# Kernel tuning notes

Measured on AMD Instinct MI355X. Metric: run time of the kernel, lower is better.

## Reference

```python
import jax, jax.numpy as jnp
import numpy as np

WIN = 9
EPS = 1e-05


def _box_sum(x, win):
    """Depthwise win x win box-filter sum with SAME padding, via two separable 1D convs."""
    C = x.shape[1]
    pad = win // 2
    dn = ('NCHW', 'OIHW', 'NCHW')
    kh = jnp.ones((C, 1, win, 1), dtype=x.dtype)
    kw = jnp.ones((C, 1, 1, win), dtype=x.dtype)
    x = jax.lax.conv_general_dilated(x, kh, (1, 1), [(pad, pad), (0, 0)],
                                     dimension_numbers=dn, feature_group_count=C)
    x = jax.lax.conv_general_dilated(x, kw, (1, 1), [(0, 0), (pad, pad)],
                                     dimension_numbers=dn, feature_group_count=C)
    return x


def setup_inputs() -> dict:
    key = jax.random.key(0)
    k1, k2 = jax.random.split(key)
    B, C, H, W = 32, 4, 512, 512
    y_pred = jax.random.uniform(k1, (B, C, H, W), dtype=jnp.float32)
    y_true = jax.random.uniform(k2, (B, C, H, W), dtype=jnp.float32)
    return {"y_pred": y_pred, "y_true": y_true}


def reference(y_pred, y_true):
    C = y_true.shape[1]
    n = float(WIN * WIN)
    # Stack the 5 moment maps along channels -> one fused box-filter pass.
    stacked = jnp.concatenate(
        [y_true, y_pred, y_true * y_true, y_pred * y_pred, y_true * y_pred], axis=1)
    sums = _box_sum(stacked, WIN)
    sum_I, sum_J, sum_I2, sum_J2, sum_IJ = jnp.split(sums, 5, axis=1)
    mu_I = sum_I / n
    mu_J = sum_J / n
    var_I = sum_I2 / n - mu_I * mu_I
    var_J = sum_J2 / n - mu_J * mu_J
    cov_IJ = sum_IJ / n - mu_I * mu_J
    cc = cov_IJ * cov_IJ / (jnp.maximum(var_I, 0.0) * jnp.maximum(var_J, 0.0) + EPS)
    return -jnp.mean(cc)
```

## Files before the change

### kernel.cpp

```cpp
#include <hip/hip_runtime.h>


#define PAD 4
#define EPS 1e-5f

constexpr int B = 32, C = 4, H = 512, W = 512;
constexpr int ROWS = 16;
constexpr int NCHUNK = H / ROWS;
constexpr int NTASK = B * C * NCHUNK;
constexpr int TPB = 256;
constexpr int WPB = TPB / 64;
constexpr int NBLK = NTASK / WPB;
constexpr float INV_N = 1.0f / 81.0f;

__device__ __forceinline__ void loadrow(const float* __restrict__ p, int r,
                                        int x0, float4& a, float4& b) {
    const float* q = p + (size_t)r * W + x0;
    a = *(const float4*)q;
    b = *(const float4*)(q + 4);
}

template <int SGN>
__device__ __forceinline__ void fold8(float s[5][8],
                                      const float4& i0, const float4& i1,
                                      const float4& j0, const float4& j1) {
    const float fi[8] = {i0.x, i0.y, i0.z, i0.w, i1.x, i1.y, i1.z, i1.w};
    const float fj[8] = {j0.x, j0.y, j0.z, j0.w, j1.x, j1.y, j1.z, j1.w};
#pragma unroll
    for (int k = 0; k < 8; ++k) {
        const float a = fi[k], b = fj[k];
        if (SGN > 0) {
            s[0][k] += a; s[1][k] += b;
            s[2][k] += a * a; s[3][k] += b * b; s[4][k] += a * b;
        } else {
            s[0][k] -= a; s[1][k] -= b;
            s[2][k] -= a * a; s[3][k] -= b * b; s[4][k] -= a * b;
        }
    }
}

template <int HALF>
__device__ __forceinline__ void hsum4(const float sc[8], int lane, float h[4]) {
    float v[12];
    if (HALF == 0) {
#pragma unroll
        for (int k = 0; k < 4; ++k) {
            const float t = __shfl_up(sc[4 + k], 1, 64);
            v[k] = (lane == 0) ? 0.0f : t;
        }
#pragma unroll
        for (int k = 0; k < 8; ++k) v[4 + k] = sc[k];
    } else {
#pragma unroll
        for (int k = 0; k < 8; ++k) v[k] = sc[k];
#pragma unroll
        for (int k = 0; k < 4; ++k) {
            const float t = __shfl_down(sc[k], 1, 64);
            v[8 + k] = (lane == 63) ? 0.0f : t;
        }
    }
    float t = v[0] + v[1] + v[2] + v[3] + v[4] + v[5] + v[6] + v[7] + v[8];
    h[0] = t;
    t += v[9]  - v[0]; h[1] = t;
    t += v[10] - v[1]; h[2] = t;
    t += v[11] - v[2]; h[3] = t;
}

__device__ __forceinline__ float cc4(const float h[5][4]) {
    float acc = 0.0f;
#pragma unroll
    for (int k = 0; k < 4; ++k) {
        const float mi = h[0][k] * INV_N;
        const float mj = h[1][k] * INV_N;
        const float vi = h[2][k] * INV_N - mi * mi;
        const float vj = h[3][k] * INV_N - mj * mj;
        const float cv = h[4][k] * INV_N - mi * mj;
        const float den = fmaxf(vi, 0.0f) * fmaxf(vj, 0.0f) + EPS;
        acc += cv * cv * __builtin_amdgcn_rcpf(den);
    }
    return acc;
}

__global__ __launch_bounds__(TPB) void ncc_partial(
        const float* __restrict__ y_pred, const float* __restrict__ y_true,
        float* __restrict__ partial) {
    const int wid = threadIdx.x >> 6;
    const int lane = threadIdx.x & 63;
    const int g = (blockIdx.x & 7) * (NBLK / 8) + (blockIdx.x >> 3);
    const int task = g * WPB + wid;
    const int plane = task >> 5;
    const int v = task & (NCHUNK - 1);
    const size_t base = (size_t)plane * H * W;
    const float* I = y_true + base;
    const float* J = y_pred + base;
    const int x0 = lane * 8;
    const int y0 = v * ROWS;

    float s[5][8];
#pragma unroll
    for (int c = 0; c < 5; ++c)
#pragma unroll
        for (int k = 0; k < 8; ++k) s[c][k] = 0.0f;

    for (int r = y0 - PAD; r <= y0 + PAD; ++r) {
        if (r < 0) continue;
        float4 i0, i1, j0, j1;
        loadrow(I, r, x0, i0, i1);
        loadrow(J, r, x0, j0, j1);
        fold8<+1>(s, i0, i1, j0, j1);
    }

    float acc = 0.0f;

    for (int yo = 0; yo < ROWS; ++yo) {
        const int y = y0 + yo;

        const int ra = y + PAD + 1;
        const bool va = (yo < ROWS - 1) && (ra < H);
        float4 ai0, ai1, aj0, aj1;
        if (va) { loadrow(I, ra, x0, ai0, ai1); loadrow(J, ra, x0, aj0, aj1); }

        const int rs = y - PAD;
        const bool vsub = (yo < ROWS - 1) && (rs >= 0);
        float4 si0, si1, sj0, sj1;
        if (vsub) { loadrow(I, rs, x0, si0, si1); loadrow(J, rs, x0, sj0, sj1); }

        {
            float h[5][4];
            hsum4<0>(s[0], lane, h[0]);
            hsum4<0>(s[1], lane, h[1]);
            hsum4<0>(s[2], lane, h[2]);
            hsum4<0>(s[3], lane, h[3]);
            hsum4<0>(s[4], lane, h[4]);
            acc += cc4(h);
        }
        {
            float h[5][4];
            hsum4<1>(s[0], lane, h[0]);
            hsum4<1>(s[1], lane, h[1]);
            hsum4<1>(s[2], lane, h[2]);
            hsum4<1>(s[3], lane, h[3]);
            hsum4<1>(s[4], lane, h[4]);
            acc += cc4(h);
        }

        if (va)   fold8<+1>(s, ai0, ai1, aj0, aj1);
        if (vsub) fold8<-1>(s, si0, si1, sj0, sj1);
    }

#pragma unroll
    for (int off = 32; off > 0; off >>= 1)
        acc += __shfl_down(acc, off, 64);
    if (lane == 0) partial[task] = acc;
}

__global__ __launch_bounds__(256) void ncc_final(
        const float* __restrict__ partial, float* __restrict__ out) {
    const int t = threadIdx.x;
    float sum = 0.0f;
    for (int i = t; i < NTASK; i += 256) sum += partial[i];
    __shared__ float ws[4];
#pragma unroll
    for (int off = 32; off > 0; off >>= 1)
        sum += __shfl_down(sum, off, 64);
    if ((t & 63) == 0) ws[t >> 6] = sum;
    __syncthreads();
    if (t == 0) {
        const float tot = ws[0] + ws[1] + ws[2] + ws[3];
        out[0] = -tot / (float)((long long)B * C * H * W);
    }
}

extern "C" void kernel_launch(void* const* d_in, const int* in_sizes, int n_in,
                              void* d_out, int out_size, void* d_ws, size_t ws_size,
                              hipStream_t stream) {
    const float* y_pred = (const float*)d_in[0];
    const float* y_true = (const float*)d_in[1];
    float* out = (float*)d_out;
    float* partial = (float*)d_ws;

    ncc_partial<<<NBLK, TPB, 0, stream>>>(y_pred, y_true, partial);
    ncc_final<<<1, 256, 0, stream>>>(partial, out);
}
```

Before: 105.7 us.

## Software-pipeline add-row loads two rows ahead and use single-wave blocks

The row loop is unrolled by two with ping-pong register buffers, so the incoming row for step yo+2 is loaded while steps yo and yo+1 compute. This hides global-load latency behind the horizontal-sum and cc work. Blocks also shrink from four wavefronts to one, with the task index taken straight from the block index. The cost is extra live registers for the prefetch buffers, which could lower occupancy, and four times as many blocks to launch.

```diff
diff --git a/kernel.cpp b/kernel.cpp
--- a/kernel.cpp
+++ b/kernel.cpp
@@ -8,9 +8,8 @@
 constexpr int ROWS = 16;
 constexpr int NCHUNK = H / ROWS;
 constexpr int NTASK = B * C * NCHUNK;
-constexpr int TPB = 256;
-constexpr int WPB = TPB / 64;
-constexpr int NBLK = NTASK / WPB;
+constexpr int TPB = 64;
+constexpr int NBLK = NTASK;
 constexpr float INV_N = 1.0f / 81.0f;
 
 __device__ __forceinline__ void loadrow(const float* __restrict__ p, int r,
@@ -81,13 +80,50 @@
     return acc;
 }
 
+#define STEP(YO, ai0, ai1, aj0, aj1)                                         \
+    {                                                                        \
+        const int y = y0 + (YO);                                             \
+        const int rs = y - PAD;                                              \
+        const bool vsub = ((YO) < ROWS - 1) && (rs >= 0);                    \
+        float4 si0, si1, sj0, sj1;                                           \
+        if (vsub) {                                                          \
+            loadrow(I, rs, x0, si0, si1);                                    \
+            loadrow(J, rs, x0, sj0, sj1);                                    \
+        }                                                                    \
+        {                                                                    \
+            float h[5][4];                                                   \
+            hsum4<0>(s[0], lane, h[0]);                                      \
+            hsum4<0>(s[1], lane, h[1]);                                      \
+            hsum4<0>(s[2], lane, h[2]);                                      \
+            hsum4<0>(s[3], lane, h[3]);                                      \
+            hsum4<0>(s[4], lane, h[4]);                                      \
+            acc += cc4(h);                                                   \
+        }                                                                    \
+        {                                                                    \
+            float h[5][4];                                                   \
+            hsum4<1>(s[0], lane, h[0]);                                      \
+            hsum4<1>(s[1], lane, h[1]);                                      \
+            hsum4<1>(s[2], lane, h[2]);                                      \
+            hsum4<1>(s[3], lane, h[3]);                                      \
+            hsum4<1>(s[4], lane, h[4]);                                      \
+            acc += cc4(h);                                                   \
+        }                                                                    \
+        const bool va = ((YO) < ROWS - 1) && (y + PAD + 1 < H);              \
+        if (va)   fold8<+1>(s, ai0, ai1, aj0, aj1);                          \
+        if (vsub) fold8<-1>(s, si0, si1, sj0, sj1);                          \
+        const int yn = (YO) + 2;                                             \
+        const int ran = y0 + yn + PAD + 1;                                   \
+        if ((yn < ROWS - 1) && (ran < H)) {                                  \
+            loadrow(I, ran, x0, ai0, ai1);                                   \
+            loadrow(J, ran, x0, aj0, aj1);                                   \
+        }                                                                    \
+    }
+
 __global__ __launch_bounds__(TPB) void ncc_partial(
         const float* __restrict__ y_pred, const float* __restrict__ y_true,
         float* __restrict__ partial) {
-    const int wid = threadIdx.x >> 6;
-    const int lane = threadIdx.x & 63;
-    const int g = (blockIdx.x & 7) * (NBLK / 8) + (blockIdx.x >> 3);
-    const int task = g * WPB + wid;
+    const int lane = threadIdx.x;
+    const int task = (blockIdx.x & 7) * (NBLK / 8) + (blockIdx.x >> 3);
     const int plane = task >> 5;
     const int v = task & (NCHUNK - 1);
     const size_t base = (size_t)plane * H * W;
@@ -110,42 +146,19 @@
         fold8<+1>(s, i0, i1, j0, j1);
     }
 
+    float4 Ai0, Ai1, Aj0, Aj1, Bi0, Bi1, Bj0, Bj1;
+    {
+        const int ra0 = y0 + PAD + 1;
+        if (ra0 < H) { loadrow(I, ra0, x0, Ai0, Ai1); loadrow(J, ra0, x0, Aj0, Aj1); }
+        const int ra1 = y0 + 1 + PAD + 1;
+        if (ra1 < H) { loadrow(I, ra1, x0, Bi0, Bi1); loadrow(J, ra1, x0, Bj0, Bj1); }
+    }
+
     float acc = 0.0f;
 
-    for (int yo = 0; yo < ROWS; ++yo) {
-        const int y = y0 + yo;
-
-        const int ra = y + PAD + 1;
-        const bool va = (yo < ROWS - 1) && (ra < H);
-        float4 ai0, ai1, aj0, aj1;
-        if (va) { loadrow(I, ra, x0, ai0, ai1); loadrow(J, ra, x0, aj0, aj1); }
-
-        const int rs = y - PAD;
-        const bool vsub = (yo < ROWS - 1) && (rs >= 0);
-        float4 si0, si1, sj0, sj1;
-        if (vsub) { loadrow(I, rs, x0, si0, si1); loadrow(J, rs, x0, sj0, sj1); }
-
-        {
-            float h[5][4];
-            hsum4<0>(s[0], lane, h[0]);
-            hsum4<0>(s[1], lane, h[1]);
-            hsum4<0>(s[2], lane, h[2]);
-            hsum4<0>(s[3], lane, h[3]);
-            hsum4<0>(s[4], lane, h[4]);
-            acc += cc4(h);
-        }
-        {
-            float h[5][4];
-            hsum4<1>(s[0], lane, h[0]);
-            hsum4<1>(s[1], lane, h[1]);
-            hsum4<1>(s[2], lane, h[2]);
-            hsum4<1>(s[3], lane, h[3]);
-            hsum4<1>(s[4], lane, h[4]);
-            acc += cc4(h);
-        }
-
-        if (va)   fold8<+1>(s, ai0, ai1, aj0, aj1);
-        if (vsub) fold8<-1>(s, si0, si1, sj0, sj1);
+    for (int yo = 0; yo < ROWS; yo += 2) {
+        STEP(yo,     Ai0, Ai1, Aj0, Aj1);
+        STEP(yo + 1, Bi0, Bi1, Bj0, Bj1);
     }
 
 #pragma unroll
```

Result: slower. 115.7 us (+9.4%).

## Compute horizontal box sums per row with halo loads instead of wave shuffles

Applied to the files above, without the earlier changes.

Each lane now loads a 16-wide halo row (neighbouring float4s) and computes the horizontal 9-tap sliding sum directly when folding a row into the vertical window. The old per-output-row cross-lane shuffles of column sums go away. In exchange, every row fold does the horizontal sliding work and 8 extra products per moment, and global loads double per row. The next add-row is also software-prefetched one iteration ahead, and the block size drops from 256 to 128 threads.

```diff
diff --git a/kernel.cpp b/kernel.cpp
--- a/kernel.cpp
+++ b/kernel.cpp
@@ -8,73 +8,77 @@
 constexpr int ROWS = 16;
 constexpr int NCHUNK = H / ROWS;
 constexpr int NTASK = B * C * NCHUNK;
-constexpr int TPB = 256;
+constexpr int TPB = 128;
 constexpr int WPB = TPB / 64;
 constexpr int NBLK = NTASK / WPB;
 constexpr float INV_N = 1.0f / 81.0f;
 
-__device__ __forceinline__ void loadrow(const float* __restrict__ p, int r,
-                                        int x0, float4& a, float4& b) {
-    const float* q = p + (size_t)r * W + x0;
-    a = *(const float4*)q;
-    b = *(const float4*)(q + 4);
+struct Row16 {
+    float4 i0, i1, i2, i3;
+    float4 j0, j1, j2, j3;
+};
+
+__device__ __forceinline__ void loadrow16(const float* __restrict__ I,
+                                          const float* __restrict__ J,
+                                          int r, int x0, bool okL, bool okR,
+                                          Row16& o) {
+    const float* pi = I + (size_t)r * W + x0;
+    const float* pj = J + (size_t)r * W + x0;
+    const float4 z = {0.f, 0.f, 0.f, 0.f};
+    o.i0 = okL ? *(const float4*)(pi - 4) : z;
+    o.i1 = *(const float4*)(pi);
+    o.i2 = *(const float4*)(pi + 4);
+    o.i3 = okR ? *(const float4*)(pi + 8) : z;
+    o.j0 = okL ? *(const float4*)(pj - 4) : z;
+    o.j1 = *(const float4*)(pj);
+    o.j2 = *(const float4*)(pj + 4);
+    o.j3 = okR ? *(const float4*)(pj + 8) : z;
 }
 
 template <int SGN>
-__device__ __forceinline__ void fold8(float s[5][8],
-                                      const float4& i0, const float4& i1,
-                                      const float4& j0, const float4& j1) {
-    const float fi[8] = {i0.x, i0.y, i0.z, i0.w, i1.x, i1.y, i1.z, i1.w};
-    const float fj[8] = {j0.x, j0.y, j0.z, j0.w, j1.x, j1.y, j1.z, j1.w};
+__device__ __forceinline__ void slide(float sh[8], const float v[16]) {
+    float t = v[0] + v[1] + v[2] + v[3] + v[4] + v[5] + v[6] + v[7] + v[8];
+    if (SGN > 0) sh[0] += t; else sh[0] -= t;
 #pragma unroll
-    for (int k = 0; k < 8; ++k) {
-        const float a = fi[k], b = fj[k];
-        if (SGN > 0) {
-            s[0][k] += a; s[1][k] += b;
-            s[2][k] += a * a; s[3][k] += b * b; s[4][k] += a * b;
-        } else {
-            s[0][k] -= a; s[1][k] -= b;
-            s[2][k] -= a * a; s[3][k] -= b * b; s[4][k] -= a * b;
-        }
+    for (int j = 1; j < 8; ++j) {
+        t += v[j + 8] - v[j - 1];
+        if (SGN > 0) sh[j] += t; else sh[j] -= t;
     }
 }
 
-template <int HALF>
-__device__ __forceinline__ void hsum4(const float sc[8], int lane, float h[4]) {
-    float v[12];
-    if (HALF == 0) {
+template <int SGN>
+__device__ __forceinline__ void foldrow(float sh[5][8], const Row16& R) {
+    const float fi[16] = {R.i0.x, R.i0.y, R.i0.z, R.i0.w,
+                          R.i1.x, R.i1.y, R.i1.z, R.i1.w,
+                          R.i2.x, R.i2.y, R.i2.z, R.i2.w,
+                          R.i3.x, R.i3.y, R.i3.z, R.i3.w};
+    const float fj[16] = {R.j0.x, R.j0.y, R.j0.z, R.j0.w,
+                          R.j1.x, R.j1.y, R.j1.z, R.j1.w,
+                          R.j2.x, R.j2.y, R.j2.z, R.j2.w,
+                          R.j3.x, R.j3.y, R.j3.z, R.j3.w};
+    slide<SGN>(sh[0], fi);
+    slide<SGN>(sh[1], fj);
+    float t[16];
 #pragma unroll
-        for (int k = 0; k < 4; ++k) {
-            const float t = __shfl_up(sc[4 + k], 1, 64);
-            v[k] = (lane == 0) ? 0.0f : t;
-        }
+    for (int c = 0; c < 16; ++c) t[c] = fi[c] * fi[c];
+    slide<SGN>(sh[2], t);
 #pragma unroll
-        for (int k = 0; k < 8; ++k) v[4 + k] = sc[k];
-    } else {
+    for (int c = 0; c < 16; ++c) t[c] = fj[c] * fj[c];
+    slide<SGN>(sh[3], t);
 #pragma unroll
-        for (int k = 0; k < 8; ++k) v[k] = sc[k];
-#pragma unroll
-        for (int k = 0; k < 4; ++k) {
-            const float t = __shfl_down(sc[k], 1, 64);
-            v[8 + k] = (lane == 63) ? 0.0f : t;
-        }
-    }
-    float t = v[0] + v[1] + v[2] + v[3] + v[4] + v[5] + v[6] + v[7] + v[8];
-    h[0] = t;
-    t += v[9]  - v[0]; h[1] = t;
-    t += v[10] - v[1]; h[2] = t;
-    t += v[11] - v[2]; h[3] = t;
+    for (int c = 0; c < 16; ++c) t[c] = fi[c] * fj[c];
+    slide<SGN>(sh[4], t);
 }
 
-__device__ __forceinline__ float cc4(const float h[5][4]) {
+__device__ __forceinline__ float cc8(const float sh[5][8]) {
     float acc = 0.0f;
 #pragma unroll
-    for (int k = 0; k < 4; ++k) {
-        const float mi = h[0][k] * INV_N;
-        const float mj = h[1][k] * INV_N;
-        const float vi = h[2][k] * INV_N - mi * mi;
-        const float vj = h[3][k] * INV_N - mj * mj;
-        const float cv = h[4][k] * INV_N - mi * mj;
+    for (int k = 0; k < 8; ++k) {
+        const float mi = sh[0][k] * INV_N;
+        const float mj = sh[1][k] * INV_N;
+        const float vi = sh[2][k] * INV_N - mi * mi;
+        const float vj = sh[3][k] * INV_N - mj * mj;
+        const float cv = sh[4][k] * INV_N - mi * mj;
         const float den = fmaxf(vi, 0.0f) * fmaxf(vj, 0.0f) + EPS;
         acc += cv * cv * __builtin_amdgcn_rcpf(den);
     }
@@ -95,57 +99,42 @@
     const float* J = y_pred + base;
     const int x0 = lane * 8;
     const int y0 = v * ROWS;
+    const bool okL = (lane != 0);
+    const bool okR = (lane != 63);
 
-    float s[5][8];
+    float sh[5][8];
 #pragma unroll
-    for (int c = 0; c < 5; ++c)
+    for (int m = 0; m < 5; ++m)
 #pragma unroll
-        for (int k = 0; k < 8; ++k) s[c][k] = 0.0f;
+        for (int j = 0; j < 8; ++j) sh[m][j] = 0.0f;
 
-    for (int r = y0 - PAD; r <= y0 + PAD; ++r) {
+    for (int r = y0 - PAD; r < y0 + PAD; ++r) {
         if (r < 0) continue;
-        float4 i0, i1, j0, j1;
-        loadrow(I, r, x0, i0, i1);
-        loadrow(J, r, x0, j0, j1);
-        fold8<+1>(s, i0, i1, j0, j1);
+        Row16 R;
+        loadrow16(I, J, r, x0, okL, okR, R);
+        foldrow<+1>(sh, R);
     }
+    Row16 A;
+    loadrow16(I, J, y0 + PAD, x0, okL, okR, A);
 
     float acc = 0.0f;
 
     for (int yo = 0; yo < ROWS; ++yo) {
         const int y = y0 + yo;
 
-        const int ra = y + PAD + 1;
-        const bool va = (yo < ROWS - 1) && (ra < H);
-        float4 ai0, ai1, aj0, aj1;
-        if (va) { loadrow(I, ra, x0, ai0, ai1); loadrow(J, ra, x0, aj0, aj1); }
+        const bool vsub = (yo < ROWS - 1) && (y - PAD >= 0);
+        Row16 S;
+        if (vsub) loadrow16(I, J, y - PAD, x0, okL, okR, S);
 
-        const int rs = y - PAD;
-        const bool vsub = (yo < ROWS - 1) && (rs >= 0);
-        float4 si0, si1, sj0, sj1;
-        if (vsub) { loadrow(I, rs, x0, si0, si1); loadrow(J, rs, x0, sj0, sj1); }
+        const bool va = (y + PAD < H);
+        if (va) foldrow<+1>(sh, A);
 
-        {
-            float h[5][4];
-            hsum4<0>(s[0], lane, h[0]);
-            hsum4<0>(s[1], lane, h[1]);
-            hsum4<0>(s[2], lane, h[2]);
-            hsum4<0>(s[3], lane, h[3]);
-            hsum4<0>(s[4], lane, h[4]);
-            acc += cc4(h);
-        }
-        {
-            float h[5][4];
-            hsum4<1>(s[0], lane, h[0]);
-            hsum4<1>(s[1], lane, h[1]);
-            hsum4<1>(s[2], lane, h[2]);
-            hsum4<1>(s[3], lane, h[3]);
-            hsum4<1>(s[4], lane, h[4]);
-            acc += cc4(h);
-        }
+        const bool vna = (yo < ROWS - 1) && (y + PAD + 1 < H);
+        if (vna) loadrow16(I, J, y + PAD + 1, x0, okL, okR, A);
 
-        if (va)   fold8<+1>(s, ai0, ai1, aj0, aj1);
-        if (vsub) fold8<-1>(s, si0, si1, sj0, sj1);
+        acc += cc8(sh);
+
+        if (vsub) foldrow<-1>(sh, S);
     }
 
 #pragma unroll
```

New measurement: 307.4 us. +190.8%, slower.
